# Optimization experiments

Hardware: AMD Instinct MI355X
Metric: run time of the kernel (lower is better)

Reference implementation:

```python
import jax, jax.numpy as jnp
import numpy as np
from jax import lax

GRAD_MUL = 0.1   # config.model.deform_conv_grad_mul
GN_GROUPS = 32
EPS = 1e-5


def conv1d(x, w, b, padding=1):
    # x [N,C,T], w [O,I,K], b [O]
    y = lax.conv_general_dilated(x, w, window_strides=(1,),
                                 padding=[(padding, padding)],
                                 dimension_numbers=('NCH', 'OIH', 'NCH'))
    return y + b[None, :, None]


def group_norm(x, gamma, beta):
    N, C, T = x.shape
    xg = x.reshape(N, GN_GROUPS, C // GN_GROUPS, T)
    mu = jnp.mean(xg, axis=(2, 3), keepdims=True)
    var = jnp.var(xg, axis=(2, 3), keepdims=True)
    xn = ((xg - mu) * lax.rsqrt(var + EPS)).reshape(N, C, T)
    return xn * gamma[None, :, None] + beta[None, :, None]


def deform_conv1d(x, off_y, w, b):
    # x [N,C,T]; off_y [N,3,T] per-tap temporal offsets; w [O,I,3]; b [O]
    # kernel=3, padding=1: tap k samples at t + (k-1) + off_y[:,k,t]
    N, C, T = x.shape
    K = 3
    base = jnp.arange(T, dtype=x.dtype)[None, None, :] + \
           (jnp.arange(K, dtype=x.dtype) - 1.0)[None, :, None]   # [1,3,T]
    pos = base + off_y                                           # [N,3,T]
    p0 = jnp.floor(pos)
    w1 = pos - p0                                                # linear interp weight
    i0 = p0.astype(jnp.int32)
    i1 = i0 + 1

    def gather(idx):
        valid = (idx >= 0) & (idx < T)                           # zero padding outside
        ic = jnp.clip(idx, 0, T - 1)
        idx_b = jnp.broadcast_to(ic[:, None, :, :], (N, C, K, T))
        x_b = jnp.broadcast_to(x[:, :, None, :], (N, C, K, T))
        g = jnp.take_along_axis(x_b, idx_b, axis=3)              # [N,C,3,T]
        return g * valid[:, None, :, :].astype(x.dtype)

    sampled = gather(i0) * (1.0 - w1)[:, None] + gather(i1) * w1[:, None]  # [N,C,3,T]
    return jnp.einsum('oik,nikt->not', w, sampled) + b[None, :, None]


def setup_inputs() -> dict:
    key = jax.random.key(0)
    ks = jax.random.split(key, 8)
    N, C, T = 8, 512, 4096
    feat = jax.random.normal(ks[0], (N, C, T), dtype=jnp.float32)
    # boundary distances in frames; scaled so offsets span multiple positions
    locs = jax.random.uniform(ks[1], (N, 2, T), dtype=jnp.float32) * 64.0
    s = 0.02
    return {
        'feat': feat,
        'locs': locs,
        'conv_w': jax.random.normal(ks[2], (C, C, 3), dtype=jnp.float32) * s,
        'conv_b': jnp.zeros((C,), dtype=jnp.float32),
        'gn_g': jnp.ones((C,), dtype=jnp.float32),
        'gn_b': jnp.zeros((C,), dtype=jnp.float32),
        'dcn_w': jax.random.normal(ks[3], (C, C, 3), dtype=jnp.float32) * s,
        'dcn_b': jnp.zeros((C,), dtype=jnp.float32),
        'out_w': jax.random.normal(ks[4], (2, C, 3), dtype=jnp.float32) * s,
        'out_b': jnp.zeros((2,), dtype=jnp.float32),
        'stride': 8,
    }


def reference(feat, locs, conv_w, conv_b, gn_g, gn_b, dcn_w, dcn_b, out_w, out_b, stride):
    # Conv1d + GroupNorm + ReLU stem (conv_layer=1)
    h = jax.nn.relu(group_norm(conv1d(feat, conv_w, conv_b), gn_g, gn_b))
    # _get_dcn_offset: gradient-scaled boundary offsets / stride
    locs_gm = ((1.0 - GRAD_MUL) * lax.stop_gradient(locs) + GRAD_MUL * locs) / jnp.float32(stride)
    y1, y2 = locs_gm[:, 0], locs_gm[:, 1]                        # [N,T]
    zero = jnp.zeros_like(y1)
    off_y = jnp.stack([-y1, zero, y2], axis=1)                   # taps 0,1,2
    offset_feat = jax.nn.relu(deform_conv1d(h, off_y, dcn_w, dcn_b))
    # Unit1D out head: Conv1d k=3 same padding, no activation
    offset = conv1d(offset_feat, out_w, out_b)
    return (offset, offset_feat)
```

## Files before the change

### kernel.cpp

```cpp
#include <hip/hip_runtime.h>
#include <hip/hip_bf16.h>

typedef __hip_bfloat16 bf16;
typedef __attribute__((ext_vector_type(8))) short short8;
typedef __attribute__((ext_vector_type(4))) float float4v;

constexpr int Nn = 8, Cc = 512, Tt = 4096, Gg = 32, CPG = 16;
constexpr float EPS = 1e-5f;

struct __align__(16) Samp { int i0, i1; float w0, w1; };

__device__ __forceinline__ float b2f(bf16 x){ return __bfloat162float(x); }
__device__ __forceinline__ bf16  f2b(float x){ return __float2bfloat16(x); }
__device__ __forceinline__ short f2s(float x){
    union { bf16 b; short s; } u; u.b = f2b(x); return u.s;
}
__device__ __forceinline__ float s2f(short x){
    union { short s; bf16 b; } u; u.s = x; return b2f(u.b);
}

__device__ __forceinline__ float stride_val(const void* sp){
    int si = *(const int*)sp;
    if (si >= 1 && si <= 100000) return (float)si;
    float sf = *(const float*)sp;
    if (sf >= 0.5f && sf <= 1.0e5f) return sf;
    return 8.0f;
}

__device__ __forceinline__ void gld16(const void* g, void* l){
    __builtin_amdgcn_global_load_lds(
        (const __attribute__((address_space(1))) unsigned int*)g,
        (__attribute__((address_space(3))) unsigned int*)l, 16, 0, 0);
}

__global__ void k_transpose(const float* __restrict__ feat, bf16* __restrict__ ftr){
    __shared__ float L[64 * 65];
    int t0 = blockIdx.x * 64, i0 = blockIdx.y * 64, n = blockIdx.z;
    int tid = threadIdx.x;
    const float* fb = feat + ((size_t)n * Cc + i0) * Tt + t0;
    #pragma unroll
    for (int it = 0; it < 4; ++it){
        int p = tid + it * 256;
        int i = p >> 4, t4 = (p & 15) * 4;
        float4v v = *(const float4v*)&fb[(size_t)i * Tt + t4];
        L[(t4 + 0) * 65 + i] = v.x;
        L[(t4 + 1) * 65 + i] = v.y;
        L[(t4 + 2) * 65 + i] = v.z;
        L[(t4 + 3) * 65 + i] = v.w;
    }
    __syncthreads();
    #pragma unroll
    for (int it = 0; it < 2; ++it){
        int p = tid + it * 256;
        int t = p >> 3, s = p & 7;
        short8 sv;
        #pragma unroll
        for (int j = 0; j < 8; ++j) sv[j] = f2s(L[t * 65 + s * 8 + j]);
        *(short8*)&ftr[((size_t)n * 4098 + t0 + t + 1) * Cc + i0 + s * 8] = sv;
    }
}

__global__ void k_zpad(bf16* __restrict__ ftr){
    int p = blockIdx.x * 256 + threadIdx.x;
    int n = p >> 10, r = (p >> 9) & 1, i = p & 511;
    ftr[((size_t)n * 4098 + (r ? 4097 : 0)) * Cc + i] = f2b(0.f);
}

__global__ void k_wcvt(const float* __restrict__ w, bf16* __restrict__ wt){
    int p = blockIdx.x * 256 + threadIdx.x;
    int k = p >> 18, rest = p & 262143;
    wt[p] = f2b(w[(size_t)rest * 3 + k]);
}


__global__ __launch_bounds__(256, 4) void k_conv1g(const bf16* __restrict__ ftr,
        const bf16* __restrict__ wtc, const float* __restrict__ bias, bf16* __restrict__ ht){
    __shared__ __align__(16) short As[128 * 32];
    __shared__ __align__(16) short Bs[128 * 32];
    __shared__ float Lt[32 * 132];
    int t0 = blockIdx.x * 128, o0 = blockIdx.y * 128, n = blockIdx.z;
    int tid = threadIdx.x, wid = tid >> 6, lane = tid & 63;
    int quad = lane >> 4, l15 = lane & 15;
    int rlo  = lane >> 2;
    int colo = 8 * ((lane & 3) ^ ((lane >> 3) & 3));
    int sgf  = 8 * (quad ^ ((lane >> 1) & 3));

    float4v acc[2][8];
    #pragma unroll
    for (int m = 0; m < 2; ++m)
        #pragma unroll
        for (int f = 0; f < 8; ++f) acc[m][f] = (float4v){0.f,0.f,0.f,0.f};

    const short* ABp = (const short*)wtc + (size_t)o0 * 512;
    const short* BBp = (const short*)ftr + ((size_t)n * 4098 + t0) * 512;
    int r0 = wid * 32;

    for (int tap = 0; tap < 3; ++tap){
        const short* Ab = ABp + (size_t)tap * 262144;
        const short* Bb = BBp + (size_t)tap * 512;
        for (int ic = 0; ic < 512; ic += 32){
            gld16(Ab + (size_t)(r0 + rlo)      * 512 + ic + colo, As + r0 * 32);
            gld16(Ab + (size_t)(r0 + 16 + rlo) * 512 + ic + colo, As + (r0 + 16) * 32);
            gld16(Bb + (size_t)(r0 + rlo)      * 512 + ic + colo, Bs + r0 * 32);
            gld16(Bb + (size_t)(r0 + 16 + rlo) * 512 + ic + colo, Bs + (r0 + 16) * 32);
            __syncthreads();
            short8 a0 = *(const short8*)&As[(r0 + l15) * 32 + sgf];
            short8 a1 = *(const short8*)&As[(r0 + 16 + l15) * 32 + sgf];
            #pragma unroll
            for (int f = 0; f < 8; ++f){
                short8 b = *(const short8*)&Bs[(f * 16 + l15) * 32 + sgf];
                acc[0][f] = __builtin_amdgcn_mfma_f32_16x16x32_bf16(a0, b, acc[0][f], 0, 0, 0);
                acc[1][f] = __builtin_amdgcn_mfma_f32_16x16x32_bf16(a1, b, acc[1][f], 0, 0, 0);
            }
            __syncthreads();
        }
    }
    #pragma unroll
    for (int pass = 0; pass < 4; ++pass){
        __syncthreads();
        #pragma unroll
        for (int m = 0; m < 2; ++m){
            #pragma unroll
            for (int fi = 0; fi < 2; ++fi){
                int f = pass * 2 + fi;
                int tl = fi * 16 + l15;
                int ob = wid * 32 + m * 16 + quad * 4;
                #pragma unroll
                for (int r = 0; r < 4; ++r)
                    Lt[tl * 132 + ob + r] = acc[m][f][r] + bias[o0 + ob + r];
            }
        }
        __syncthreads();
        #pragma unroll
        for (int it = 0; it < 2; ++it){
            int p = tid + it * 256;
            int tl = p >> 4, s = p & 15;
            short8 sv;
            #pragma unroll
            for (int j = 0; j < 8; ++j) sv[j] = f2s(Lt[tl * 132 + s * 8 + j]);
            *(short8*)&ht[((size_t)n * Tt + t0 + pass * 32 + tl) * Cc + o0 + s * 8] = sv;
        }
    }
}

__global__ void k_gnstats2(const bf16* __restrict__ ht, float* __restrict__ mean,
                           float* __restrict__ rstd){
    int blk = blockIdx.x;
    int n = blk >> 5, g = blk & 31;
    const bf16* base = ht + (size_t)n * Tt * Cc + g * 16 + (threadIdx.x & 1) * 8;
    float s = 0.f, ss = 0.f;
    for (int r = threadIdx.x >> 1; r < Tt; r += 128){
        short8 v = *(const short8*)&base[(size_t)r * Cc];
        #pragma unroll
        for (int j = 0; j < 8; ++j){ float f = s2f(v[j]); s += f; ss += f * f; }
    }
    __shared__ float sh[512];
    sh[threadIdx.x] = s; sh[256 + threadIdx.x] = ss;
    __syncthreads();
    for (int off = 128; off > 0; off >>= 1){
        if (threadIdx.x < off){
            sh[threadIdx.x] += sh[threadIdx.x + off];
            sh[256 + threadIdx.x] += sh[256 + threadIdx.x + off];
        }
        __syncthreads();
    }
    if (threadIdx.x == 0){
        float m = sh[0] / (float)(CPG * Tt);
        float v = sh[256] / (float)(CPG * Tt) - m * m;
        mean[blk] = m; rstd[blk] = rsqrtf(v + EPS);
    }
}

__global__ void k_gnapply2(bf16* __restrict__ ht, const float* __restrict__ mean,
        const float* __restrict__ rstd, const float* __restrict__ gamma,
        const float* __restrict__ beta){
    int p = blockIdx.x * 256 + threadIdx.x;
    int s = p & 63, row = p >> 6;
    int n = row >> 12;
    int ib = s * 8;
    int blk = n * 32 + (ib >> 4);
    float mu = mean[blk], rs = rstd[blk];
    short8 v = *(short8*)&ht[(size_t)row * Cc + ib];
    short8 o;
    #pragma unroll
    for (int j = 0; j < 8; ++j){
        int c = ib + j;
        float f = (s2f(v[j]) - mu) * rs * gamma[c] + beta[c];
        o[j] = f2s(fmaxf(f, 0.f));
    }
    *(short8*)&ht[(size_t)row * Cc + ib] = o;
}

__global__ void k_prep(const float* __restrict__ locs, const void* __restrict__ sp,
        Samp* __restrict__ pa, Samp* __restrict__ pc){
    int idx = blockIdx.x * 256 + threadIdx.x;
    int t = idx & 4095, n = idx >> 12;
    float s = stride_val(sp);
    float l1 = locs[((size_t)n * 2 + 0) * Tt + t];
    float l2 = locs[((size_t)n * 2 + 1) * Tt + t];
    float y1 = (0.9f * l1 + 0.1f * l1) / s;
    float y2 = (0.9f * l2 + 0.1f * l2) / s;
    float pos0 = (float)(t - 1) - y1;
    float pos2 = (float)(t + 1) + y2;
    float p0f = floorf(pos0), p2f = floorf(pos2);
    float w1 = pos0 - p0f, w2 = pos2 - p2f;
    int a0 = (int)p0f, a1 = a0 + 1, c0 = (int)p2f, c1 = c0 + 1;
    Samp A, C;
    A.w0 = (a0 >= 0 && a0 < Tt) ? (1.f - w1) : 0.f;
    A.w1 = (a1 >= 0 && a1 < Tt) ? w1 : 0.f;
    C.w0 = (c0 >= 0 && c0 < Tt) ? (1.f - w2) : 0.f;
    C.w1 = (c1 >= 0 && c1 < Tt) ? w2 : 0.f;
    A.i0 = min(max(a0, 0), Tt - 1);
    A.i1 = min(max(a1, 0), Tt - 1);
    C.i0 = min(max(c0, 0), Tt - 1);
    C.i1 = min(max(c1, 0), Tt - 1);
    pa[idx] = A;
    pc[idx] = C;
}

__global__ __launch_bounds__(256, 4) void k_deformg(const bf16* __restrict__ ht,
        const Samp* __restrict__ pa, const Samp* __restrict__ pc,
        const bf16* __restrict__ wtd, const float* __restrict__ bias,
        float* __restrict__ out){
    __shared__ __align__(16) short As[128 * 32];
    __shared__ __align__(16) short Bs[128 * 32];
    int t0 = blockIdx.x * 128, o0 = blockIdx.y * 128, n = blockIdx.z;
    int tid = threadIdx.x, wid = tid >> 6, lane = tid & 63;
    int quad = lane >> 4, l15 = lane & 15;
    int rlo  = lane >> 2;
    int slot = lane & 3;
    int colo = 8 * (slot ^ ((rlo >> 1) & 3));
    int sgf  = 8 * (quad ^ ((lane >> 1) & 3));
    int r0 = wid * 32;

    float4v acc[2][8];
    #pragma unroll
    for (int m = 0; m < 2; ++m)
        #pragma unroll
        for (int f = 0; f < 8; ++f) acc[m][f] = (float4v){0.f,0.f,0.f,0.f};

    int row_a = r0 + rlo, row_b = r0 + 16 + rlo;
    size_t pbase = (size_t)n * Tt + t0;
    Samp sa0 = pa[pbase + row_a];
    Samp sa1 = pa[pbase + row_b];
    Samp sc0 = pc[pbase + row_a];
    Samp sc1 = pc[pbase + row_b];

    const short* hs = (const short*)ht + (size_t)n * Tt * 512;
    const short* ga0 = hs + (size_t)sa0.i0 * 512 + colo;
    const short* ga1 = hs + (size_t)sa0.i1 * 512 + colo;
    const short* gb0 = hs + (size_t)sa1.i0 * 512 + colo;
    const short* gb1 = hs + (size_t)sa1.i1 * 512 + colo;
    const short* gc0 = hs + (size_t)sc0.i0 * 512 + colo;
    const short* gc1 = hs + (size_t)sc0.i1 * 512 + colo;
    const short* gd0 = hs + (size_t)sc1.i0 * 512 + colo;
    const short* gd1 = hs + (size_t)sc1.i1 * 512 + colo;

    const short* Bb1 = hs + (size_t)t0 * 512;
    const short* ABp = (const short*)wtd + (size_t)o0 * 512;

    for (int tap = 0; tap < 3; ++tap){
        const short* Ab = ABp + (size_t)tap * 262144;
        for (int ic = 0; ic < 512; ic += 32){
            gld16(Ab + (size_t)(r0 + rlo)      * 512 + ic + colo, As + r0 * 32);
            gld16(Ab + (size_t)(r0 + 16 + rlo) * 512 + ic + colo, As + (r0 + 16) * 32);
            if (tap == 1){
                gld16(Bb1 + (size_t)(r0 + rlo)      * 512 + ic + colo, Bs + r0 * 32);
                gld16(Bb1 + (size_t)(r0 + 16 + rlo) * 512 + ic + colo, Bs + (r0 + 16) * 32);
            } else {
                const short* p0 = (tap == 0) ? ga0 : gc0;
                const short* p1 = (tap == 0) ? ga1 : gc1;
                const short* q0 = (tap == 0) ? gb0 : gd0;
                const short* q1 = (tap == 0) ? gb1 : gd1;
                float w00 = (tap == 0) ? sa0.w0 : sc0.w0;
                float w01 = (tap == 0) ? sa0.w1 : sc0.w1;
                float w10 = (tap == 0) ? sa1.w0 : sc1.w0;
                float w11 = (tap == 0) ? sa1.w1 : sc1.w1;
                short8 lo0 = *(const short8*)&p0[ic];
                short8 hi0 = *(const short8*)&p1[ic];
                short8 lo1 = *(const short8*)&q0[ic];
                short8 hi1 = *(const short8*)&q1[ic];
                short8 o0, o1;
                #pragma unroll
                for (int j = 0; j < 8; ++j){
                    o0[j] = f2s(w00 * s2f(lo0[j]) + w01 * s2f(hi0[j]));
                    o1[j] = f2s(w10 * s2f(lo1[j]) + w11 * s2f(hi1[j]));
                }
                *(short8*)&Bs[row_a * 32 + slot * 8] = o0;
                *(short8*)&Bs[row_b * 32 + slot * 8] = o1;
            }
            __syncthreads();
            short8 a0 = *(const short8*)&As[(r0 + l15) * 32 + sgf];
            short8 a1 = *(const short8*)&As[(r0 + 16 + l15) * 32 + sgf];
            #pragma unroll
            for (int f = 0; f < 8; ++f){
                short8 b = *(const short8*)&Bs[(f * 16 + l15) * 32 + sgf];
                acc[0][f] = __builtin_amdgcn_mfma_f32_16x16x32_bf16(a0, b, acc[0][f], 0, 0, 0);
                acc[1][f] = __builtin_amdgcn_mfma_f32_16x16x32_bf16(a1, b, acc[1][f], 0, 0, 0);
            }
            __syncthreads();
        }
    }
    float* ob = out + (size_t)n * Cc * Tt;
    #pragma unroll
    for (int m = 0; m < 2; ++m){
        int ob0 = o0 + wid * 32 + m * 16 + quad * 4;
        #pragma unroll
        for (int r = 0; r < 4; ++r){
            float bs = bias[ob0 + r];
            size_t row = (size_t)(ob0 + r) * Tt;
            #pragma unroll
            for (int f = 0; f < 8; ++f)
                ob[row + t0 + f * 16 + l15] = fmaxf(acc[m][f][r] + bs, 0.f);
        }
    }
}

__global__ void k_outinit(const float* __restrict__ ob, float* __restrict__ out){
    int idx = blockIdx.x * 256 + threadIdx.x;
    out[idx] = ob[(idx >> 12) & 1];
}

__global__ void k_outconv(const float* __restrict__ x, const float* __restrict__ w,
                          float* __restrict__ out){
    int t  = blockIdx.x * 256 + threadIdx.x;
    int i0 = blockIdx.y * 64;
    int n  = blockIdx.z;
    const float* xb = x + (size_t)n * Cc * Tt;
    float a0 = 0.f, a1 = 0.f;
    bool tm = (t > 0), tp = (t < Tt - 1);
    for (int i = i0; i < i0 + 64; ++i){
        const float* xr = xb + (size_t)i * Tt + t;
        float xm = tm ? xr[-1] : 0.f;
        float x0 = xr[0];
        float xp = tp ? xr[1] : 0.f;
        const float* w0 = w + i * 3;
        const float* w1 = w + Cc * 3 + i * 3;
        a0 += xm * w0[0] + x0 * w0[1] + xp * w0[2];
        a1 += xm * w1[0] + x0 * w1[1] + xp * w1[2];
    }
    atomicAdd(&out[((size_t)n * 2 + 0) * Tt + t], a0);
    atomicAdd(&out[((size_t)n * 2 + 1) * Tt + t], a1);
}

extern "C" void kernel_launch(void* const* d_in, const int* in_sizes, int n_in,
                              void* d_out, int out_size, void* d_ws, size_t ws_size,
                              hipStream_t stream) {
    const float* feat   = (const float*)d_in[0];
    const float* locs   = (const float*)d_in[1];
    const float* conv_w = (const float*)d_in[2];
    const float* conv_b = (const float*)d_in[3];
    const float* gn_g   = (const float*)d_in[4];
    const float* gn_b   = (const float*)d_in[5];
    const float* dcn_w  = (const float*)d_in[6];
    const float* dcn_b  = (const float*)d_in[7];
    const float* out_w  = (const float*)d_in[8];
    const float* out_b  = (const float*)d_in[9];

    float* offset      = (float*)d_out;
    float* offset_feat = (float*)d_out + (size_t)Nn * 2 * Tt;

    constexpr size_t OFF_PREP = 4096;
    constexpr size_t SZ_SAMP  = (size_t)32768 * sizeof(Samp);
    constexpr size_t OFF_WTC  = OFF_PREP + 2 * SZ_SAMP;
    constexpr size_t OFF_WTD  = OFF_WTC + 3 * 512 * 512 * 2;
    constexpr size_t OFF_FTR  = OFF_WTD + 3 * 512 * 512 * 2;
    constexpr size_t OFF_HT   = OFF_FTR + (size_t)8 * 4098 * 512 * 2;

    float* mean = (float*)d_ws;
    float* rstd = (float*)((char*)d_ws + 1024);

    char* ws = (char*)d_ws;
    Samp* pa  = (Samp*)(ws + OFF_PREP);
    Samp* pc  = (Samp*)(ws + OFF_PREP + SZ_SAMP);
    bf16* wtc = (bf16*)(ws + OFF_WTC);
    bf16* wtd = (bf16*)(ws + OFF_WTD);
    bf16* ftr = (bf16*)(ws + OFF_FTR);
    bf16* ht  = (bf16*)(ws + OFF_HT);

    k_transpose<<<dim3(64, 8, 8), 256, 0, stream>>>(feat, ftr);
    k_zpad     <<<32, 256, 0, stream>>>(ftr);
    k_wcvt     <<<3072, 256, 0, stream>>>(conv_w, wtc);
    k_wcvt     <<<3072, 256, 0, stream>>>(dcn_w, wtd);
    k_conv1g   <<<dim3(32, 4, 8), 256, 0, stream>>>(ftr, wtc, conv_b, ht);
    k_gnstats2 <<<256, 256, 0, stream>>>(ht, mean, rstd);
    k_gnapply2 <<<8192, 256, 0, stream>>>(ht, mean, rstd, gn_g, gn_b);
    k_prep     <<<128, 256, 0, stream>>>(locs, d_in[10], pa, pc);
    k_deformg  <<<dim3(32, 4, 8), 256, 0, stream>>>(ht, pa, pc, wtd, dcn_b, offset_feat);
    k_outinit  <<<256, 256, 0, stream>>>(out_b, offset);
    k_outconv  <<<dim3(16, 8, 8), 256, 0, stream>>>(offset_feat, out_w, offset);
}
```

Baseline: 335.3 us.

## Double-buffer LDS tiles in deformable GEMM and prefetch next chunk during MFMA

Splits the A and B shared-memory tiles into two buffers and flattens the tap/channel loops into a single 48-step loop. Each step issues the weight and plain-tap loads for the next chunk, and the gathered loads and bilinear interpolation for the offset taps, while MFMAs run on the current buffer. This drops one barrier per iteration and aims to hide global gather latency behind compute. The cost is double the LDS footprint (32KB per block), which may reduce occupancy, plus extra registers for the prefetched values.

```diff
diff --git a/kernel.cpp b/kernel.cpp
--- a/kernel.cpp
+++ b/kernel.cpp
@@ -222,8 +222,8 @@
         const Samp* __restrict__ pa, const Samp* __restrict__ pc,
         const bf16* __restrict__ wtd, const float* __restrict__ bias,
         float* __restrict__ out){
-    __shared__ __align__(16) short As[128 * 32];
-    __shared__ __align__(16) short Bs[128 * 32];
+    __shared__ __align__(16) short As[2][128 * 32];
+    __shared__ __align__(16) short Bs[2][128 * 32];
     int t0 = blockIdx.x * 128, o0 = blockIdx.y * 128, n = blockIdx.z;
     int tid = threadIdx.x, wid = tid >> 6, lane = tid & 63;
     int quad = lane >> 4, l15 = lane & 15;
@@ -259,48 +259,77 @@
     const short* Bb1 = hs + (size_t)t0 * 512;
     const short* ABp = (const short*)wtd + (size_t)o0 * 512;
 
-    for (int tap = 0; tap < 3; ++tap){
-        const short* Ab = ABp + (size_t)tap * 262144;
-        for (int ic = 0; ic < 512; ic += 32){
-            gld16(Ab + (size_t)(r0 + rlo)      * 512 + ic + colo, As + r0 * 32);
-            gld16(Ab + (size_t)(r0 + 16 + rlo) * 512 + ic + colo, As + (r0 + 16) * 32);
-            if (tap == 1){
-                gld16(Bb1 + (size_t)(r0 + rlo)      * 512 + ic + colo, Bs + r0 * 32);
-                gld16(Bb1 + (size_t)(r0 + 16 + rlo) * 512 + ic + colo, Bs + (r0 + 16) * 32);
-            } else {
-                const short* p0 = (tap == 0) ? ga0 : gc0;
-                const short* p1 = (tap == 0) ? ga1 : gc1;
-                const short* q0 = (tap == 0) ? gb0 : gd0;
-                const short* q1 = (tap == 0) ? gb1 : gd1;
-                float w00 = (tap == 0) ? sa0.w0 : sc0.w0;
-                float w01 = (tap == 0) ? sa0.w1 : sc0.w1;
-                float w10 = (tap == 0) ? sa1.w0 : sc1.w0;
-                float w11 = (tap == 0) ? sa1.w1 : sc1.w1;
-                short8 lo0 = *(const short8*)&p0[ic];
-                short8 hi0 = *(const short8*)&p1[ic];
-                short8 lo1 = *(const short8*)&q0[ic];
-                short8 hi1 = *(const short8*)&q1[ic];
-                short8 o0, o1;
-                #pragma unroll
-                for (int j = 0; j < 8; ++j){
-                    o0[j] = f2s(w00 * s2f(lo0[j]) + w01 * s2f(hi0[j]));
-                    o1[j] = f2s(w10 * s2f(lo1[j]) + w11 * s2f(hi1[j]));
-                }
-                *(short8*)&Bs[row_a * 32 + slot * 8] = o0;
-                *(short8*)&Bs[row_b * 32 + slot * 8] = o1;
+    {
+        short8 lo0 = *(const short8*)&ga0[0];
+        short8 hi0 = *(const short8*)&ga1[0];
+        short8 lo1 = *(const short8*)&gb0[0];
+        short8 hi1 = *(const short8*)&gb1[0];
+        gld16(ABp + (size_t)(r0 + rlo)      * 512 + colo, &As[0][r0 * 32]);
+        gld16(ABp + (size_t)(r0 + 16 + rlo) * 512 + colo, &As[0][(r0 + 16) * 32]);
+        short8 o0v, o1v;
+        #pragma unroll
+        for (int j = 0; j < 8; ++j){
+            o0v[j] = f2s(sa0.w0 * s2f(lo0[j]) + sa0.w1 * s2f(hi0[j]));
+            o1v[j] = f2s(sa1.w0 * s2f(lo1[j]) + sa1.w1 * s2f(hi1[j]));
+        }
+        *(short8*)&Bs[0][row_a * 32 + slot * 8] = o0v;
+        *(short8*)&Bs[0][row_b * 32 + slot * 8] = o1v;
+    }
+    __syncthreads();
+
+    #pragma unroll 2
+    for (int ch = 0; ch < 48; ++ch){
+        int cur = ch & 1, nxt = cur ^ 1;
+        int chn = ch + 1;
+        int tapn = chn >> 4, icn = (chn & 15) << 5;
+        short8 lo0n, hi0n, lo1n, hi1n;
+        float w00 = 0.f, w01 = 0.f, w10 = 0.f, w11 = 0.f;
+        bool pre_lerp = false;
+        if (chn < 48){
+            if (tapn != 1){
+                const short* p0 = (tapn == 0) ? ga0 : gc0;
+                const short* p1 = (tapn == 0) ? ga1 : gc1;
+                const short* q0 = (tapn == 0) ? gb0 : gd0;
+                const short* q1 = (tapn == 0) ? gb1 : gd1;
+                w00 = (tapn == 0) ? sa0.w0 : sc0.w0;
+                w01 = (tapn == 0) ? sa0.w1 : sc0.w1;
+                w10 = (tapn == 0) ? sa1.w0 : sc1.w0;
+                w11 = (tapn == 0) ? sa1.w1 : sc1.w1;
+                lo0n = *(const short8*)&p0[icn];
+                hi0n = *(const short8*)&p1[icn];
+                lo1n = *(const short8*)&q0[icn];
+                hi1n = *(const short8*)&q1[icn];
+                pre_lerp = true;
             }
-            __syncthreads();
-            short8 a0 = *(const short8*)&As[(r0 + l15) * 32 + sgf];
-            short8 a1 = *(const short8*)&As[(r0 + 16 + l15) * 32 + sgf];
+            const short* Abn = ABp + (size_t)tapn * 262144;
+            gld16(Abn + (size_t)(r0 + rlo)      * 512 + icn + colo, &As[nxt][r0 * 32]);
+            gld16(Abn + (size_t)(r0 + 16 + rlo) * 512 + icn + colo, &As[nxt][(r0 + 16) * 32]);
+            if (tapn == 1){
+                gld16(Bb1 + (size_t)(r0 + rlo)      * 512 + icn + colo, &Bs[nxt][r0 * 32]);
+                gld16(Bb1 + (size_t)(r0 + 16 + rlo) * 512 + icn + colo, &Bs[nxt][(r0 + 16) * 32]);
+            }
+        }
+        short8 a0 = *(const short8*)&As[cur][(r0 + l15) * 32 + sgf];
+        short8 a1 = *(const short8*)&As[cur][(r0 + 16 + l15) * 32 + sgf];
+        #pragma unroll
+        for (int f = 0; f < 8; ++f){
+            short8 b = *(const short8*)&Bs[cur][(f * 16 + l15) * 32 + sgf];
+            acc[0][f] = __builtin_amdgcn_mfma_f32_16x16x32_bf16(a0, b, acc[0][f], 0, 0, 0);
+            acc[1][f] = __builtin_amdgcn_mfma_f32_16x16x32_bf16(a1, b, acc[1][f], 0, 0, 0);
+        }
+        if (pre_lerp){
+            short8 o0v, o1v;
             #pragma unroll
-            for (int f = 0; f < 8; ++f){
-                short8 b = *(const short8*)&Bs[(f * 16 + l15) * 32 + sgf];
-                acc[0][f] = __builtin_amdgcn_mfma_f32_16x16x32_bf16(a0, b, acc[0][f], 0, 0, 0);
-                acc[1][f] = __builtin_amdgcn_mfma_f32_16x16x32_bf16(a1, b, acc[1][f], 0, 0, 0);
+            for (int j = 0; j < 8; ++j){
+                o0v[j] = f2s(w00 * s2f(lo0n[j]) + w01 * s2f(hi0n[j]));
+                o1v[j] = f2s(w10 * s2f(lo1n[j]) + w11 * s2f(hi1n[j]));
             }
-            __syncthreads();
-        }
-    }
+            *(short8*)&Bs[nxt][row_a * 32 + slot * 8] = o0v;
+            *(short8*)&Bs[nxt][row_b * 32 + slot * 8] = o1v;
+        }
+        __syncthreads();
+    }
+
     float* ob = out + (size_t)n * Cc * Tt;
     #pragma unroll
     for (int m = 0; m < 2; ++m){
```

New measurement: 362.1 us. 8.0% more time.
